# Kernel tuning notes

Measured on AMD Instinct MI355X. Metric: run time of the kernel, lower is better.

Reference implementation:

```python
import jax, jax.numpy as jnp
import numpy as np

IMG = 640.0
NC = 20
LAMBDA_BOX, LAMBDA_OBJ, LAMBDA_CLS = 0.05, 1.0, 0.5
ANCHORS = jnp.array([[10,13],[16,30],[33,23],[30,61],[62,45],[59,119],[116,90],[156,198],[373,326]], dtype=jnp.float32) / IMG
SCALES = [(80,80),(40,40),(20,20)]


def build_target(boxes, labels, scale_idx):
    # boxes: (N,M,4) [x1,y1,x2,y2] in pixels; labels: (N,M) int
    H, W = SCALES[scale_idx]
    anc = ANCHORS[scale_idx*3:(scale_idx+1)*3]            # (3,2)
    N, M, _ = boxes.shape
    x1, y1, x2, y2 = boxes[...,0], boxes[...,1], boxes[...,2], boxes[...,3]
    valid = (x2 > x1) & (y2 > y1)                          # skip degenerate boxes
    cx = (x1 + x2) / 2.0 / IMG
    cy = (y1 + y2) / 2.0 / IMG
    w  = (x2 - x1) / IMG
    h  = (y2 - y1) / IMG
    gx = jnp.floor(cx * W).astype(jnp.int32)               # int() truncation (coords >=0)
    gy = jnp.floor(cy * H).astype(jnp.int32)
    dx = cx * W - gx
    dy = cy * H - gy
    rw = w[..., None] / anc[:, 0]                          # (N,M,3)
    rh = h[..., None] / anc[:, 1]
    ious = jnp.minimum(rw, 1.0/rw) * jnp.minimum(rh, 1.0/rh)
    best = jnp.argmax(ious, axis=-1)                       # (N,M)
    aw, ah = anc[best, 0], anc[best, 1]
    tw = jnp.log(w / aw + 1e-6)
    th = jnp.log(h / ah + 1e-6)
    onehot = jax.nn.one_hot(labels, NC, dtype=boxes.dtype) # (N,M,NC)
    vec = jnp.concatenate([jnp.stack([dx, dy, tw, th, jnp.ones_like(dx)], axis=-1), onehot], axis=-1)  # (N,M,5+NC)
    # route invalid boxes out of range -> dropped by scatter
    gy_s = jnp.where(valid, gy, -1)
    gx_s = jnp.where(valid, gx, -1)
    b = jnp.broadcast_to(jnp.arange(N)[:, None], (N, M))
    ch = jnp.arange(5 + NC)
    t = jnp.zeros((N, 3, 5 + NC, H, W), boxes.dtype)
    t = t.at[b[..., None], best[..., None], ch[None, None, :], gy_s[..., None], gx_s[..., None]].set(vec, mode='drop')
    return t


def bce_with_logits_mean(x, t):
    return jnp.mean(jnp.maximum(x, 0.0) - x * t + jnp.log1p(jnp.exp(-jnp.abs(x))))


def bbox_iou(b1, b2, eps=1e-7):
    # b1,b2: (...,4) center format [cx,cy,w,h]
    b1x1 = b1[...,0]-b1[...,2]/2; b1y1 = b1[...,1]-b1[...,3]/2
    b1x2 = b1[...,0]+b1[...,2]/2; b1y2 = b1[...,1]+b1[...,3]/2
    b2x1 = b2[...,0]-b2[...,2]/2; b2y1 = b2[...,1]-b2[...,3]/2
    b2x2 = b2[...,0]+b2[...,2]/2; b2y2 = b2[...,1]+b2[...,3]/2
    iw = jnp.clip(jnp.minimum(b1x2, b2x2) - jnp.maximum(b1x1, b2x1), 0.0)
    ih = jnp.clip(jnp.minimum(b1y2, b2y2) - jnp.maximum(b1y1, b2y1), 0.0)
    inter = iw * ih
    union = (b1x2-b1x1)*(b1y2-b1y1) + (b2x2-b2x1)*(b2y2-b2y1) - inter + eps
    return inter / union


def yolo_loss(preds, boxes, labels, scale_idx):
    H, W = SCALES[scale_idx]
    stride = IMG / H
    A = 3
    anc = ANCHORS[scale_idx*A:(scale_idx+1)*A]
    target = build_target(boxes, labels, scale_idx)        # (N,A,5+NC,H,W)
    preds = preds.reshape(-1, A, 5 + NC, H, W)
    p_obj = preds[:, :, 4]
    p_cls = preds[:, :, 5:]
    t_obj = target[:, :, 4]
    t_cls = target[:, :, 5:]
    ygrid, xgrid = jnp.meshgrid(jnp.arange(H), jnp.arange(W), indexing='ij')
    grid = jnp.stack((xgrid, ygrid), 2).reshape(1, 1, H, W, 2).astype(preds.dtype)
    p_txty = jnp.transpose(preds[:, :, 0:2], (0, 1, 3, 4, 2))   # (N,A,H,W,2)
    p_twth = jnp.transpose(preds[:, :, 2:4], (0, 1, 3, 4, 2))
    p_xy = (2.0 * jax.nn.sigmoid(p_txty) - 0.5 + grid) * stride
    p_wh = (2.0 * jax.nn.sigmoid(p_twth)) ** 2 * anc.reshape(1, A, 1, 1, 2)
    p_box = jnp.concatenate([p_xy, p_wh], axis=-1)
    t_txty = jnp.transpose(target[:, :, 0:2], (0, 1, 3, 4, 2))
    t_twth = jnp.transpose(target[:, :, 2:4], (0, 1, 3, 4, 2))
    t_xy = (t_txty + grid) * stride
    t_wh = jnp.exp(t_twth) * anc.reshape(1, A, 1, 1, 2)
    t_box = jnp.concatenate([t_xy, t_wh], axis=-1)
    pos = (t_obj == 1.0).astype(preds.dtype)                   # (N,A,H,W)
    iou_sum = jnp.sum(bbox_iou(p_box, t_box) * pos)
    loss_box = 1.0 - iou_sum
    loss_obj = bce_with_logits_mean(p_obj, t_obj)
    loss_cls = bce_with_logits_mean(p_cls, t_cls)
    return LAMBDA_BOX * loss_box + LAMBDA_OBJ * loss_obj + LAMBDA_CLS * loss_cls


def setup_inputs() -> dict:
    key = jax.random.key(0)
    k1, k2, k3 = jax.random.split(key, 3)
    N, M = 64, 40
    preds = jax.random.normal(k1, (N, 3, 5 + NC, 80, 80), dtype=jnp.float32)
    # sample corner pairs in [0,640) and sort so x1<x2, y1<y2
    xy = jnp.sort(jax.random.uniform(k2, (N, M, 2, 2), minval=0.0, maxval=640.0), axis=-1)
    boxes = jnp.stack([xy[..., 0, 0], xy[..., 1, 0], xy[..., 0, 1], xy[..., 1, 1]], axis=-1)
    labels = jax.random.randint(k3, (N, M), 0, NC, dtype=jnp.int32)
    return {"preds": preds, "boxes": boxes, "labels": labels, "scale_idx": 0}


def reference(preds, boxes, labels, scale_idx):
    return yolo_loss(preds, boxes, labels, scale_idx)
```

## Files before the change

### kernel.cpp

```cpp
#include <hip/hip_runtime.h>
#include <math.h>

namespace {
constexpr int kNImg = 64;
constexpr int kM    = 40;
constexpr int kA    = 3;
constexpr int kNC   = 20;
constexpr int kH    = 80;
constexpr int kW    = 80;
constexpr int kHW   = kH * kW;
constexpr int kHW4  = kHW / 4;
constexpr int kC    = 5 + kNC;
constexpr int kPPF4 = kC * kHW4;
constexpr int kVPP  = (1 + kNC) * kHW4;
constexpr int kNV   = kNImg * kA * kVPP;
constexpr double kInvObj = 1.0 / 1228800.0;
constexpr double kInvCls = 1.0 / 24576000.0;
constexpr int kGrid = 1024;
}

__device__ __forceinline__ float wave_red(float v) {
#pragma unroll
  for (int o = 32; o > 0; o >>= 1) v += __shfl_down(v, o, 64);
  return v;
}

__device__ __forceinline__ float softplus_fast(float x) {
  return fmaxf(x, 0.0f) + __logf(1.0f + __expf(-fabsf(x)));
}

__global__ __launch_bounds__(256) void yolo_fused(
    const float* __restrict__ preds, const float* __restrict__ boxes,
    const int* __restrict__ labels, float* __restrict__ out, int nblocks) {
  __shared__ int s_keys[64];
  __shared__ float s_red[4][5];
  const int tid = threadIdx.x;
  const int bid = blockIdx.x;

  float sp_obj = 0.0f, sp_cls = 0.0f;
  const float4* __restrict__ pv = (const float4*)preds;
  const int stride = nblocks * 256;
  int i = bid * 256 + tid;
  for (; i + 3 * stride < kNV; i += 4 * stride) {
    int idx[4];
    float4 v[4];
#pragma unroll
    for (int u = 0; u < 4; ++u) idx[u] = i + u * stride;
#pragma unroll
    for (int u = 0; u < 4; ++u) {
      int plane = idx[u] / kVPP;
      int rem = idx[u] - plane * kVPP;
      v[u] = pv[plane * kPPF4 + 4 * kHW4 + rem];
      idx[u] = rem;
    }
#pragma unroll
    for (int u = 0; u < 4; ++u) {
      float s = softplus_fast(v[u].x) + softplus_fast(v[u].y) +
                softplus_fast(v[u].z) + softplus_fast(v[u].w);
      if (idx[u] < kHW4) sp_obj += s;
      else sp_cls += s;
    }
  }
  for (; i < kNV; i += stride) {
    int plane = i / kVPP;
    int rem = i - plane * kVPP;
    float4 v = pv[plane * kPPF4 + 4 * kHW4 + rem];
    float s = softplus_fast(v.x) + softplus_fast(v.y) + softplus_fast(v.z) +
              softplus_fast(v.w);
    if (rem < kHW4) sp_obj += s;
    else sp_cls += s;
  }

  float corr_obj = 0.0f, corr_cls = 0.0f, iou_acc = 0.0f;
  int mykey = -1, best = 0, gx = 0, gy = 0, lab = 0;
  float dx = 0.0f, dy = 0.0f, twv = 0.0f, thv = 0.0f;

  const float ancw[3] = {10.0f / 640.0f, 16.0f / 640.0f, 33.0f / 640.0f};
  const float anch[3] = {13.0f / 640.0f, 30.0f / 640.0f, 23.0f / 640.0f};

  if (bid < kNImg && tid < 64) {
    int key = -1;
    if (tid < kM) {
      const float* bp = boxes + ((bid * kM + tid) << 2);
      float x1 = bp[0], y1 = bp[1], x2 = bp[2], y2 = bp[3];
      bool valid = (x2 > x1) && (y2 > y1);
      float cx = ((x1 + x2) * 0.5f) / 640.0f;
      float cy = ((y1 + y2) * 0.5f) / 640.0f;
      float w = (x2 - x1) / 640.0f;
      float h = (y2 - y1) / 640.0f;
      float fx = cx * (float)kW;
      float fy = cy * (float)kH;
      gx = (int)floorf(fx);
      gy = (int)floorf(fy);
      dx = fx - (float)gx;
      dy = fy - (float)gy;
      float bestv = -1e30f;
      int b = 0;
#pragma unroll
      for (int a = 0; a < 3; ++a) {
        float rw = w / ancw[a];
        float rh = h / anch[a];
        float i1 = fminf(rw, 1.0f / rw) * fminf(rh, 1.0f / rh);
        if (i1 > bestv) { bestv = i1; b = a; }
      }
      best = b;
      twv = logf(w / ancw[b] + 1e-6f);
      thv = logf(h / anch[b] + 1e-6f);
      lab = labels[bid * kM + tid];
      if (valid && gx >= 0 && gx < kW && gy >= 0 && gy < kH)
        key = (b * kH + gy) * kW + gx;
    }
    s_keys[tid] = key;
    mykey = key;
  }
  __syncthreads();

  if (mykey >= 0) {
    bool win = true;
    for (int mp = tid + 1; mp < kM; ++mp)
      if (s_keys[mp] == mykey) { win = false; break; }
    if (win) {
      const float* pp =
          preds + (size_t)(bid * kA + best) * kC * kHW + (gy * kW + gx);
      float xtx = pp[0];
      float xty = pp[kHW];
      float xtw = pp[2 * kHW];
      float xth = pp[3 * kHW];
      float xob = pp[4 * kHW];
      float xcl = pp[(5 + lab) * kHW];
      corr_obj = -xob;
      corr_cls = -xcl;
      float aw = ancw[best], ah = anch[best];
      float sx = 1.0f / (1.0f + expf(-xtx));
      float sy = 1.0f / (1.0f + expf(-xty));
      float sw = 1.0f / (1.0f + expf(-xtw));
      float sh = 1.0f / (1.0f + expf(-xth));
      float px = (2.0f * sx - 0.5f + (float)gx) * 8.0f;
      float py = (2.0f * sy - 0.5f + (float)gy) * 8.0f;
      float pw = (2.0f * sw) * (2.0f * sw) * aw;
      float ph = (2.0f * sh) * (2.0f * sh) * ah;
      float tx = (dx + (float)gx) * 8.0f;
      float ty = (dy + (float)gy) * 8.0f;
      float tw2 = expf(twv) * aw;
      float th2 = expf(thv) * ah;
      float b1x1 = px - pw * 0.5f, b1x2 = px + pw * 0.5f;
      float b1y1 = py - ph * 0.5f, b1y2 = py + ph * 0.5f;
      float b2x1 = tx - tw2 * 0.5f, b2x2 = tx + tw2 * 0.5f;
      float b2y1 = ty - th2 * 0.5f, b2y2 = ty + th2 * 0.5f;
      float iw = fmaxf(fminf(b1x2, b2x2) - fmaxf(b1x1, b2x1), 0.0f);
      float ih = fmaxf(fminf(b1y2, b2y2) - fmaxf(b1y1, b2y1), 0.0f);
      float inter = iw * ih;
      float uni = (b1x2 - b1x1) * (b1y2 - b1y1) +
                  (b2x2 - b2x1) * (b2y2 - b2y1) - inter + 1e-7f;
      iou_acc = inter / uni;
    }
  }

  float vals[5] = {sp_obj, sp_cls, corr_obj, corr_cls, iou_acc};
#pragma unroll
  for (int j = 0; j < 5; ++j) vals[j] = wave_red(vals[j]);
  const int wid = tid >> 6, lane = tid & 63;
  if (lane == 0) {
#pragma unroll
    for (int j = 0; j < 5; ++j) s_red[wid][j] = vals[j];
  }
  __syncthreads();
  if (tid == 0) {
    double t[5];
#pragma unroll
    for (int j = 0; j < 5; ++j)
      t[j] = (double)s_red[0][j] + (double)s_red[1][j] +
             (double)s_red[2][j] + (double)s_red[3][j];
    double contrib = (t[0] + t[2]) * kInvObj +
                     0.5 * (t[1] + t[3]) * kInvCls - 0.05 * t[4];
    if (bid == 0) contrib += 0.05;
    atomicAdd(out, (float)contrib);
  }
}

extern "C" void kernel_launch(void* const* d_in, const int* in_sizes, int n_in,
                              void* d_out, int out_size, void* d_ws,
                              size_t ws_size, hipStream_t stream) {
  const float* preds = (const float*)d_in[0];
  const float* boxes = (const float*)d_in[1];
  const int* labels = (const int*)d_in[2];
  float* out = (float*)d_out;
  (void)d_ws; (void)ws_size;

  yolo_fused<<<kGrid, 256, 0, stream>>>(preds, boxes, labels, out, kGrid);
}
```

Before: 182.5 us.

## Fold loss scaling into a single accumulator and use nontemporal loads

Replaces the five separate per-thread accumulators with one scaled float accumulator, applying the obj/cls normalisation inside the streaming loop, and does the final block sum in float instead of double. The main streaming loop now uses nontemporal vector loads with a 2-way unroll instead of 4, and the target-matching work moves ahead of the stream. The aim is to cut reduction work, register pressure and cache pollution. It trades away some summation precision and memory-level parallelism.

```diff
diff --git a/kernel.cpp b/kernel.cpp
--- a/kernel.cpp
+++ b/kernel.cpp
@@ -14,10 +14,12 @@
 constexpr int kPPF4 = kC * kHW4;
 constexpr int kVPP  = (1 + kNC) * kHW4;
 constexpr int kNV   = kNImg * kA * kVPP;
-constexpr double kInvObj = 1.0 / 1228800.0;
-constexpr double kInvCls = 1.0 / 24576000.0;
+constexpr float kInvObjF  = 1.0f / 1228800.0f;
+constexpr float kHInvClsF = 0.5f / 24576000.0f;
 constexpr int kGrid = 1024;
 }
+
+typedef float f4v __attribute__((ext_vector_type(4)));
 
 __device__ __forceinline__ float wave_red(float v) {
 #pragma unroll
@@ -33,50 +35,17 @@
     const float* __restrict__ preds, const float* __restrict__ boxes,
     const int* __restrict__ labels, float* __restrict__ out, int nblocks) {
   __shared__ int s_keys[64];
-  __shared__ float s_red[4][5];
+  __shared__ float s_red[4];
   const int tid = threadIdx.x;
   const int bid = blockIdx.x;
 
-  float sp_obj = 0.0f, sp_cls = 0.0f;
-  const float4* __restrict__ pv = (const float4*)preds;
-  const int stride = nblocks * 256;
-  int i = bid * 256 + tid;
-  for (; i + 3 * stride < kNV; i += 4 * stride) {
-    int idx[4];
-    float4 v[4];
-#pragma unroll
-    for (int u = 0; u < 4; ++u) idx[u] = i + u * stride;
-#pragma unroll
-    for (int u = 0; u < 4; ++u) {
-      int plane = idx[u] / kVPP;
-      int rem = idx[u] - plane * kVPP;
-      v[u] = pv[plane * kPPF4 + 4 * kHW4 + rem];
-      idx[u] = rem;
-    }
-#pragma unroll
-    for (int u = 0; u < 4; ++u) {
-      float s = softplus_fast(v[u].x) + softplus_fast(v[u].y) +
-                softplus_fast(v[u].z) + softplus_fast(v[u].w);
-      if (idx[u] < kHW4) sp_obj += s;
-      else sp_cls += s;
-    }
-  }
-  for (; i < kNV; i += stride) {
-    int plane = i / kVPP;
-    int rem = i - plane * kVPP;
-    float4 v = pv[plane * kPPF4 + 4 * kHW4 + rem];
-    float s = softplus_fast(v.x) + softplus_fast(v.y) + softplus_fast(v.z) +
-              softplus_fast(v.w);
-    if (rem < kHW4) sp_obj += s;
-    else sp_cls += s;
-  }
-
-  float corr_obj = 0.0f, corr_cls = 0.0f, iou_acc = 0.0f;
-  int mykey = -1, best = 0, gx = 0, gy = 0, lab = 0;
-  float dx = 0.0f, dy = 0.0f, twv = 0.0f, thv = 0.0f;
+  float acc = 0.0f;
 
   const float ancw[3] = {10.0f / 640.0f, 16.0f / 640.0f, 33.0f / 640.0f};
   const float anch[3] = {13.0f / 640.0f, 30.0f / 640.0f, 23.0f / 640.0f};
+
+  int mykey = -1, best = 0, gx = 0, gy = 0, lab = 0;
+  float dx = 0.0f, dy = 0.0f, twv = 0.0f, thv = 0.0f;
 
   if (bid < kNImg && tid < 64) {
     int key = -1;
@@ -128,8 +97,6 @@
       float xth = pp[3 * kHW];
       float xob = pp[4 * kHW];
       float xcl = pp[(5 + lab) * kHW];
-      corr_obj = -xob;
-      corr_cls = -xcl;
       float aw = ancw[best], ah = anch[best];
       float sx = 1.0f / (1.0f + expf(-xtx));
       float sy = 1.0f / (1.0f + expf(-xty));
@@ -152,29 +119,42 @@
       float inter = iw * ih;
       float uni = (b1x2 - b1x1) * (b1y2 - b1y1) +
                   (b2x2 - b2x1) * (b2y2 - b2y1) - inter + 1e-7f;
-      iou_acc = inter / uni;
+      float iou = inter / uni;
+      acc = -xob * kInvObjF - xcl * kHInvClsF - 0.05f * iou;
     }
   }
 
-  float vals[5] = {sp_obj, sp_cls, corr_obj, corr_cls, iou_acc};
-#pragma unroll
-  for (int j = 0; j < 5; ++j) vals[j] = wave_red(vals[j]);
-  const int wid = tid >> 6, lane = tid & 63;
-  if (lane == 0) {
-#pragma unroll
-    for (int j = 0; j < 5; ++j) s_red[wid][j] = vals[j];
+  const f4v* __restrict__ pv = (const f4v*)preds;
+  const int stride = nblocks * 256;
+  int i = bid * 256 + tid;
+  for (; i + stride < kNV; i += 2 * stride) {
+    int i1 = i + stride;
+    int p0 = i / kVPP, r0 = i - p0 * kVPP;
+    int p1 = i1 / kVPP, r1 = i1 - p1 * kVPP;
+    f4v v0 = __builtin_nontemporal_load(pv + (p0 * kPPF4 + 4 * kHW4 + r0));
+    f4v v1 = __builtin_nontemporal_load(pv + (p1 * kPPF4 + 4 * kHW4 + r1));
+    float s0 = softplus_fast(v0.x) + softplus_fast(v0.y) +
+               softplus_fast(v0.z) + softplus_fast(v0.w);
+    float s1 = softplus_fast(v1.x) + softplus_fast(v1.y) +
+               softplus_fast(v1.z) + softplus_fast(v1.w);
+    acc = fmaf(s0, (r0 < kHW4) ? kInvObjF : kHInvClsF, acc);
+    acc = fmaf(s1, (r1 < kHW4) ? kInvObjF : kHInvClsF, acc);
   }
+  if (i < kNV) {
+    int p0 = i / kVPP, r0 = i - p0 * kVPP;
+    f4v v0 = __builtin_nontemporal_load(pv + (p0 * kPPF4 + 4 * kHW4 + r0));
+    float s0 = softplus_fast(v0.x) + softplus_fast(v0.y) +
+               softplus_fast(v0.z) + softplus_fast(v0.w);
+    acc = fmaf(s0, (r0 < kHW4) ? kInvObjF : kHInvClsF, acc);
+  }
+
+  acc = wave_red(acc);
+  if ((tid & 63) == 0) s_red[tid >> 6] = acc;
   __syncthreads();
   if (tid == 0) {
-    double t[5];
-#pragma unroll
-    for (int j = 0; j < 5; ++j)
-      t[j] = (double)s_red[0][j] + (double)s_red[1][j] +
-             (double)s_red[2][j] + (double)s_red[3][j];
-    double contrib = (t[0] + t[2]) * kInvObj +
-                     0.5 * (t[1] + t[3]) * kInvCls - 0.05 * t[4];
-    if (bid == 0) contrib += 0.05;
-    atomicAdd(out, (float)contrib);
+    float b = s_red[0] + s_red[1] + s_red[2] + s_red[3];
+    if (bid == 0) b += 0.05f;
+    atomicAdd(out, b);
   }
 }
 
```

Result: faster. 176.0 us (-3.6%).
